# Kernel tuning notes

Measured on AMD Instinct MI355X. Metric: run time of the kernel, lower is better.

Reference implementation:

```python
import jax, jax.numpy as jnp
import numpy as np

B, S, H, NH = 8, 1024, 1024, 4
D = H // NH
NEG = jnp.float32(-2**32 + 1)


def setup_inputs() -> dict:
    key = jax.random.key(0)
    ks = jax.random.split(key, 12)
    w = 1.0 / np.sqrt(H)
    wf = 1.0 / np.sqrt(2 * H)
    return {
        "memory": jax.random.normal(ks[0], (B, S, H), jnp.float32),
        "decoder_input": jax.random.normal(ks[1], (B, S, H), jnp.float32),
        "mask": jax.random.bernoulli(ks[2], 0.2, (B, S, S)),
        "query_mask": (jax.random.uniform(ks[3], (B, S)) > 0.1).astype(jnp.float32),
        "Wk": jax.random.normal(ks[4], (H, H), jnp.float32) * w,
        "Wv": jax.random.normal(ks[5], (H, H), jnp.float32) * w,
        "Wq": jax.random.normal(ks[6], (H, H), jnp.float32) * w,
        "Wf": jax.random.normal(ks[7], (2 * H, H), jnp.float32) * wf,
        "bf": jnp.zeros((H,), jnp.float32),
        "gamma": jnp.ones((H,), jnp.float32),
        "beta": jnp.zeros((H,), jnp.float32),
        "g_factor": jax.random.uniform(ks[8], (1,), jnp.float32, 1e4, 2e4),
    }


def reference(memory, decoder_input, mask, query_mask, Wk, Wv, Wq, Wf, bf, gamma, beta, g_factor):
    b, sq, hdim = decoder_input.shape
    sk = memory.shape[1]

    def heads(x, W, s):  # -> (NH, B, s, D), matching torch permute(2,0,1,3)
        return (x @ W).reshape(b, s, NH, D).transpose(2, 0, 1, 3)

    k = heads(memory, Wk, sk)
    v = heads(memory, Wv, sk)
    q = heads(decoder_input, Wq, sq)

    attn = jnp.einsum("hbqd,hbkd->hbqk", q, k) / jnp.sqrt(jnp.float32(D))
    idx = jnp.arange(sk, dtype=jnp.float32)
    gauss = (idx[:, None] - idx[None, :]) ** 2 / g_factor[0]  # (sq, sk), sq==sk
    attn = attn - gauss
    attn = jnp.where(mask[None], NEG, attn)
    attn = jax.nn.softmax(attn, axis=-1)
    attn = attn * query_mask[None, :, :, None]  # post-softmax query mask

    res = jnp.einsum("hbqk,hbkd->hbqd", attn, v)
    res = res.transpose(1, 2, 0, 3).reshape(b, sq, hdim)

    out = jnp.concatenate([decoder_input, res], axis=-1) @ Wf + bf
    out = out + decoder_input
    mu = out.mean(-1, keepdims=True)
    var = ((out - mu) ** 2).mean(-1, keepdims=True)
    out = (out - mu) / jnp.sqrt(var + 1e-5) * gamma + beta
    return out, attn.reshape(NH * b, sq, sk)
```

## Files before the change

### kernel.cpp

```cpp
#include <hip/hip_runtime.h>

#define B_ 8
#define S_ 1024
#define H_ 1024
#define NH_ 4
#define D_ 256
#define M_ 8192

typedef unsigned int u32;
typedef unsigned short u16;
typedef __attribute__((ext_vector_type(4))) float f32x4;
typedef __attribute__((ext_vector_type(8))) short s16x8;

__device__ __forceinline__ float bf2f(u16 b) { return __uint_as_float(((u32)b) << 16); }
__device__ __forceinline__ u16 f2bf(float f) {
    u32 x = __float_as_uint(f);
    return (u16)((x + 0x7fffu + ((x >> 16) & 1u)) >> 16);
}

__global__ void init_flags_k(int* fl) { fl[0] = 0; fl[1] = 0; fl[2] = 0; }

__global__ __launch_bounds__(256) void or_mask_k(const u32* __restrict__ m, int* __restrict__ fl) {
    u32 v = m[blockIdx.x * 256 + threadIdx.x];
#pragma unroll
    for (int o = 32; o; o >>= 1) v |= __shfl_xor(v, o, 64);
    if ((threadIdx.x & 63) == 0) atomicOr(fl + 1, (int)v);
}

__global__ void classify_mask_k(int* fl) {
    u32 R = (u32)fl[1];
    int c;
    if (R == 0x3F803F80u)      c = 2;
    else if (R == 0x3F800000u) c = 3;
    else if (R & 0xFFFFFF00u)  c = 0;
    else                       c = 1;
    fl[2] = c;
}

__global__ __launch_bounds__(256) void tcast_k(const float* __restrict__ src, u16* __restrict__ dst,
                                               int R, int C) {
    __shared__ float sb[32][33];
    const int c0 = blockIdx.x * 32, r0 = blockIdx.y * 32;
    const int tx = threadIdx.x & 31, ty = threadIdx.x >> 5;
#pragma unroll
    for (int i = 0; i < 4; i++)
        sb[ty + 8 * i][tx] = src[(size_t)(r0 + ty + 8 * i) * C + c0 + tx];
    __syncthreads();
#pragma unroll
    for (int i = 0; i < 4; i++)
        dst[(size_t)(c0 + ty + 8 * i) * R + r0 + tx] = f2bf(sb[tx][ty + 8 * i]);
}

__global__ __launch_bounds__(256) void castbf_k(const float* __restrict__ src, u16* __restrict__ dst) {
    const int i = blockIdx.x * 256 + threadIdx.x;
    float4 v = ((const float4*)src)[i];
    ushort4 o;
    o.x = f2bf(v.x); o.y = f2bf(v.y); o.z = f2bf(v.z); o.w = f2bf(v.w);
    ((ushort4*)dst)[i] = o;
}

template<int AMODE>
__device__ __forceinline__ void gemm_core(
    const float* __restrict__ A32, const u16* __restrict__ A16, int lda,
    const u16* __restrict__ Bp, int ldb, int K, int m0, int n0,
    short* As, short* Bs, f32x4 acc[4][4])
{
    const int t = threadIdx.x;
    const int lane = t & 63, wave = t >> 6;
    const int wy = wave >> 1, wx = wave & 1;
    const int mq = lane >> 4, ml = lane & 15;
    const int srow = t >> 2, skq = t & 3;

    for (int k0 = 0; k0 < K; k0 += 32) {
        __syncthreads();
#pragma unroll
        for (int it = 0; it < 2; it++) {
            const int row = srow + it * 64;
            const int kk = k0 + skq * 8;
            short* dst = As + row * 40 + skq * 8;
            if (AMODE == 1) {
                *(s16x8*)dst = *(const s16x8*)(A16 + (size_t)(m0 + row) * lda + kk);
            } else {
                if (kk < 1024) {
                    const float* s = A32 + (size_t)(m0 + row) * 1024 + kk;
                    float4 v0 = *(const float4*)s, v1 = *(const float4*)(s + 4);
                    s16x8 p;
                    p[0] = (short)f2bf(v0.x); p[1] = (short)f2bf(v0.y);
                    p[2] = (short)f2bf(v0.z); p[3] = (short)f2bf(v0.w);
                    p[4] = (short)f2bf(v1.x); p[5] = (short)f2bf(v1.y);
                    p[6] = (short)f2bf(v1.z); p[7] = (short)f2bf(v1.w);
                    *(s16x8*)dst = p;
                } else {
                    *(s16x8*)dst = *(const s16x8*)(A16 + (size_t)(m0 + row) * 1024 + (kk - 1024));
                }
            }
        }
#pragma unroll
        for (int it = 0; it < 2; it++) {
            const int row = srow + it * 64;
            *(s16x8*)(Bs + row * 40 + skq * 8) =
                *(const s16x8*)(Bp + (size_t)(n0 + row) * ldb + k0 + skq * 8);
        }
        __syncthreads();
        s16x8 af[4], bfr[4];
#pragma unroll
        for (int i = 0; i < 4; i++) {
            af[i]  = *(s16x8*)(As + (wy * 64 + i * 16 + ml) * 40 + mq * 8);
            bfr[i] = *(s16x8*)(Bs + (wx * 64 + i * 16 + ml) * 40 + mq * 8);
        }
#pragma unroll
        for (int mi = 0; mi < 4; mi++)
#pragma unroll
            for (int ni = 0; ni < 4; ni++)
                acc[mi][ni] = __builtin_amdgcn_mfma_f32_16x16x32_bf16(af[mi], bfr[ni], acc[mi][ni], 0, 0, 0);
    }
}

__global__ __launch_bounds__(256) void gemm_proj_k(const u16* __restrict__ A, const u16* __restrict__ WT,
                                                   u16* __restrict__ C) {
    __shared__ short As[128 * 40];
    __shared__ short Bs[128 * 40];
    const int m0 = blockIdx.y * 128, n0 = blockIdx.x * 128;
    f32x4 acc[4][4];
#pragma unroll
    for (int i = 0; i < 4; i++)
#pragma unroll
        for (int j = 0; j < 4; j++) acc[i][j] = 0;
    gemm_core<1>(nullptr, A, H_, WT, H_, H_, m0, n0, As, Bs, acc);
    const int lane = threadIdx.x & 63, wave = threadIdx.x >> 6;
    const int wy = wave >> 1, wx = wave & 1, mq = lane >> 4, ml = lane & 15;
#pragma unroll
    for (int mi = 0; mi < 4; mi++)
#pragma unroll
        for (int ni = 0; ni < 4; ni++) {
            const int n = n0 + wx * 64 + ni * 16 + ml;
#pragma unroll
            for (int r = 0; r < 4; r++) {
                const int m = m0 + wy * 64 + mi * 16 + mq * 4 + r;
                C[(size_t)m * H_ + n] = f2bf(acc[mi][ni][r]);
            }
        }
}

__global__ __launch_bounds__(256) void gemm_vt_k(const u16* __restrict__ A, const u16* __restrict__ WT,
                                                 u16* __restrict__ VT) {
    __shared__ short As[128 * 40];
    __shared__ short Bs[128 * 40];
    const int m0 = blockIdx.y * 128, n0 = blockIdx.x * 128;
    f32x4 acc[4][4];
#pragma unroll
    for (int i = 0; i < 4; i++)
#pragma unroll
        for (int j = 0; j < 4; j++) acc[i][j] = 0;
    gemm_core<1>(nullptr, A, H_, WT, H_, H_, m0, n0, As, Bs, acc);
    const int lane = threadIdx.x & 63, wave = threadIdx.x >> 6;
    const int wy = wave >> 1, wx = wave & 1, mq = lane >> 4, ml = lane & 15;
#pragma unroll
    for (int mi = 0; mi < 4; mi++)
#pragma unroll
        for (int ni = 0; ni < 4; ni++) {
            const int n = n0 + wx * 64 + ni * 16 + ml;
            const int mbase = m0 + wy * 64 + mi * 16 + mq * 4;
            const int b = mbase >> 10, s = mbase & 1023;
            ushort4 w;
            w.x = f2bf(acc[mi][ni][0]); w.y = f2bf(acc[mi][ni][1]);
            w.z = f2bf(acc[mi][ni][2]); w.w = f2bf(acc[mi][ni][3]);
            *(ushort4*)(VT + ((size_t)(b * 1024 + n)) * 1024 + s) = w;
        }
}

__global__ __launch_bounds__(512, 2) void qk_sm_k(
    const u16* __restrict__ Qb, const u16* __restrict__ Kb,
    const void* __restrict__ mask, const float* __restrict__ gfac,
    const int* __restrict__ fl, const float* __restrict__ qmask,
    float* __restrict__ attn, const u16* __restrict__ VT, u16* __restrict__ resB)
{
    __shared__ short smem[76288];
    short* As = smem;
    short* Bs = smem + 2560;
    short* Ps = smem;
    short* Vs = smem + 65536;
    float* red = (float*)(smem + 75776);

    const int flat = blockIdx.x;
    const int wgid = (flat & 7) * 64 + (flat >> 3);
    const int z = wgid >> 4, m0 = (wgid & 15) * 64;
    const int h = z >> 3, b = z & 7;

    const u16* Aq = Qb + (size_t)b * S_ * H_ + h * D_;
    const u16* Bk = Kb + (size_t)b * S_ * H_ + h * D_;

    const int t = threadIdx.x;
    const int lane = t & 63, wave = t >> 6;
    const int wm = wave >> 2, wn = wave & 3;
    const int mq = lane >> 4, ml = lane & 15;

    f32x4 acc[2][16];
#pragma unroll
    for (int mi = 0; mi < 2; mi++)
#pragma unroll
        for (int nf = 0; nf < 16; nf++) acc[mi][nf] = 0;

    for (int k0 = 0; k0 < D_; k0 += 32) {
        __syncthreads();
        if (t < 256) {
            const int row = t >> 2, kq = t & 3;
            *(s16x8*)(As + row * 40 + kq * 8) =
                *(const s16x8*)(Aq + (size_t)(m0 + row) * H_ + k0 + kq * 8);
        }
#pragma unroll
        for (int it = 0; it < 8; it++) {
            const int c = it * 512 + t;
            const int row = c >> 2, kq = c & 3;
            *(s16x8*)(Bs + row * 40 + kq * 8) =
                *(const s16x8*)(Bk + (size_t)row * H_ + k0 + kq * 8);
        }
        __syncthreads();
        s16x8 af0 = *(s16x8*)(As + (wm * 32 + ml) * 40 + mq * 8);
        s16x8 af1 = *(s16x8*)(As + (wm * 32 + 16 + ml) * 40 + mq * 8);
#pragma unroll
        for (int g4 = 0; g4 < 4; g4++) {
            s16x8 bf4[4];
#pragma unroll
            for (int j = 0; j < 4; j++)
                bf4[j] = *(s16x8*)(Bs + (wn * 256 + (g4 * 4 + j) * 16 + ml) * 40 + mq * 8);
#pragma unroll
            for (int j = 0; j < 4; j++) {
                acc[0][g4 * 4 + j] = __builtin_amdgcn_mfma_f32_16x16x32_bf16(af0, bf4[j], acc[0][g4 * 4 + j], 0, 0, 0);
                acc[1][g4 * 4 + j] = __builtin_amdgcn_mfma_f32_16x16x32_bf16(af1, bf4[j], acc[1][g4 * 4 + j], 0, 0, 0);
            }
        }
    }

    const float ginv = 1.0f / gfac[0];
    const int code = fl[2];
    const size_t zrow = (size_t)z * S_;
    float rmax[2][4], rsum[2][4], scv[2][4];

#pragma unroll
    for (int mi = 0; mi < 2; mi++)
#pragma unroll
        for (int r = 0; r < 4; r++) {
            const int qg = m0 + wm * 32 + mi * 16 + mq * 4 + r;
            const size_t mbase = ((size_t)b * S_ + qg) * S_;
            float mx = -3.0e38f;
#pragma unroll
            for (int nf = 0; nf < 16; nf++) {
                const int kg = wn * 256 + nf * 16 + ml;
                float diff = (float)(qg - kg);
                float val = acc[mi][nf][r] * 0.0625f - diff * diff * ginv;
                int mv;
                if (code == 0)      mv = ((const unsigned char*)mask)[mbase + kg];
                else if (code == 1) mv = ((const int*)mask)[mbase + kg];
                else if (code == 2) mv = (((const u16*)mask)[mbase + kg] != 0);
                else                mv = (((const u32*)mask)[mbase + kg] != 0);
                if (mv) val = -4294967296.0f;
                acc[mi][nf][r] = val;
                mx = fmaxf(mx, val);
            }
            rmax[mi][r] = mx;
        }
#pragma unroll
    for (int o = 1; o < 16; o <<= 1)
#pragma unroll
        for (int mi = 0; mi < 2; mi++)
#pragma unroll
            for (int r = 0; r < 4; r++)
                rmax[mi][r] = fmaxf(rmax[mi][r], __shfl_xor(rmax[mi][r], o, 64));
    if (ml == 0)
#pragma unroll
        for (int mi = 0; mi < 2; mi++)
#pragma unroll
            for (int r = 0; r < 4; r++) red[(wm * 32 + mi * 16 + mq * 4 + r) * 4 + wn] = rmax[mi][r];
    __syncthreads();
#pragma unroll
    for (int mi = 0; mi < 2; mi++)
#pragma unroll
        for (int r = 0; r < 4; r++) {
            const float* rr = red + (wm * 32 + mi * 16 + mq * 4 + r) * 4;
            rmax[mi][r] = fmaxf(fmaxf(rr[0], rr[1]), fmaxf(rr[2], rr[3]));
        }
    __syncthreads();
#pragma unroll
    for (int mi = 0; mi < 2; mi++)
#pragma unroll
        for (int r = 0; r < 4; r++) {
            float s = 0.f;
#pragma unroll
            for (int nf = 0; nf < 16; nf++) {
                float p = __expf(acc[mi][nf][r] - rmax[mi][r]);
                acc[mi][nf][r] = p;
                s += p;
            }
            rsum[mi][r] = s;
        }
#pragma unroll
    for (int o = 1; o < 16; o <<= 1)
#pragma unroll
        for (int mi = 0; mi < 2; mi++)
#pragma unroll
            for (int r = 0; r < 4; r++) rsum[mi][r] += __shfl_xor(rsum[mi][r], o, 64);
    if (ml == 0)
#pragma unroll
        for (int mi = 0; mi < 2; mi++)
#pragma unroll
            for (int r = 0; r < 4; r++) red[(wm * 32 + mi * 16 + mq * 4 + r) * 4 + wn] = rsum[mi][r];
    __syncthreads();
#pragma unroll
    for (int mi = 0; mi < 2; mi++)
#pragma unroll
        for (int r = 0; r < 4; r++) {
            const float* rr = red + (wm * 32 + mi * 16 + mq * 4 + r) * 4;
            const int qg = m0 + wm * 32 + mi * 16 + mq * 4 + r;
            const float s = rr[0] + rr[1] + rr[2] + rr[3];
            scv[mi][r] = qmask[b * S_ + qg] / s;
        }

#pragma unroll
    for (int mi = 0; mi < 2; mi++)
#pragma unroll
        for (int r = 0; r < 4; r++) {
            const int prow = wm * 32 + mi * 16 + mq * 4 + r;
            const int qg = m0 + prow;
            float* gp = attn + (zrow + qg) * S_ + wn * 256 + ml;
            const float sc = scv[mi][r];
#pragma unroll
            for (int nf = 0; nf < 16; nf++) {
                const float v = acc[mi][nf][r] * sc;
                gp[nf * 16] = v;
                const int col = wn * 256 + nf * 16 + ml;
                Ps[prow * 1024 + (col ^ ((prow & 7) << 3))] = (short)f2bf(v);
            }
        }

    const int wr = wave >> 2, wc = wave & 3;
    f32x4 acc2[2][4];
#pragma unroll
    for (int mi = 0; mi < 2; mi++)
#pragma unroll
        for (int ni = 0; ni < 4; ni++) acc2[mi][ni] = 0;

    const u16* Vp = VT + ((size_t)(b * 1024 + h * D_)) * 1024;
    for (int k0 = 0; k0 < S_; k0 += 32) {
        {
            const int row = t >> 1, half = t & 1;
            const u16* s = Vp + (size_t)row * 1024 + k0 + half * 16;
            short* dpt = Vs + row * 40 + half * 16;
            *(s16x8*)dpt       = *(const s16x8*)s;
            *(s16x8*)(dpt + 8) = *(const s16x8*)(s + 8);
        }
        __syncthreads();
        s16x8 pa[2];
#pragma unroll
        for (int mi = 0; mi < 2; mi++) {
            const int prow = wr * 32 + mi * 16 + ml;
            pa[mi] = *(s16x8*)(Ps + prow * 1024 + ((((k0 >> 3) + mq) ^ (prow & 7)) << 3));
        }
#pragma unroll
        for (int ni = 0; ni < 4; ni++) {
            s16x8 vf = *(s16x8*)(Vs + (wc * 64 + ni * 16 + ml) * 40 + mq * 8);
            acc2[0][ni] = __builtin_amdgcn_mfma_f32_16x16x32_bf16(pa[0], vf, acc2[0][ni], 0, 0, 0);
            acc2[1][ni] = __builtin_amdgcn_mfma_f32_16x16x32_bf16(pa[1], vf, acc2[1][ni], 0, 0, 0);
        }
        __syncthreads();
    }

    u16* C = resB + (size_t)b * S_ * H_ + h * D_;
#pragma unroll
    for (int mi = 0; mi < 2; mi++)
#pragma unroll
        for (int ni = 0; ni < 4; ni++) {
            const int n = wc * 64 + ni * 16 + ml;
#pragma unroll
            for (int r = 0; r < 4; r++) {
                const int m = m0 + wr * 32 + mi * 16 + mq * 4 + r;
                C[(size_t)m * H_ + n] = f2bf(acc2[mi][ni][r]);
            }
        }
}

__global__ __launch_bounds__(256) void final_mfma_k(const float* __restrict__ dec, const u16* __restrict__ resB,
                                                    const u16* __restrict__ WfT, const float* __restrict__ bfv,
                                                    u16* __restrict__ tmp) {
    __shared__ short As[128 * 40];
    __shared__ short Bs[128 * 40];
    const int m0 = blockIdx.y * 128, n0 = blockIdx.x * 128;
    f32x4 acc[4][4];
#pragma unroll
    for (int i = 0; i < 4; i++)
#pragma unroll
        for (int j = 0; j < 4; j++) acc[i][j] = 0;
    gemm_core<2>(dec, resB, H_, WfT, 2048, 2048, m0, n0, As, Bs, acc);
    const int lane = threadIdx.x & 63, wave = threadIdx.x >> 6;
    const int wy = wave >> 1, wx = wave & 1, mq = lane >> 4, ml = lane & 15;
#pragma unroll
    for (int mi = 0; mi < 4; mi++)
#pragma unroll
        for (int ni = 0; ni < 4; ni++) {
            const int n = n0 + wx * 64 + ni * 16 + ml;
#pragma unroll
            for (int r = 0; r < 4; r++) {
                const int m = m0 + wy * 64 + mi * 16 + mq * 4 + r;
                float val = acc[mi][ni][r] + bfv[n] + dec[(size_t)m * H_ + n];
                tmp[(size_t)m * H_ + n] = f2bf(val);
            }
        }
}

__global__ __launch_bounds__(256) void ln2_k(const u16* __restrict__ tmp, const float* __restrict__ gm,
                                             const float* __restrict__ bt, float* __restrict__ out) {
    const int m = blockIdx.x, t = threadIdx.x;
    ushort4 u = ((const ushort4*)(tmp + (size_t)m * H_))[t];
    float xa[4] = {bf2f(u.x), bf2f(u.y), bf2f(u.z), bf2f(u.w)};
    float s = 0.f, s2 = 0.f;
#pragma unroll
    for (int i = 0; i < 4; i++) { s += xa[i]; s2 += xa[i] * xa[i]; }
#pragma unroll
    for (int o = 32; o; o >>= 1) { s += __shfl_xor(s, o, 64); s2 += __shfl_xor(s2, o, 64); }
    __shared__ float rs[4], rs2[4];
    if ((t & 63) == 0) { rs[t >> 6] = s; rs2[t >> 6] = s2; }
    __syncthreads();
    s  = rs[0] + rs[1] + rs[2] + rs[3];
    s2 = rs2[0] + rs2[1] + rs2[2] + rs2[3];
    float mu = s * (1.f / 1024.f);
    float var = s2 * (1.f / 1024.f) - mu * mu;
    float rstd = rsqrtf(var + 1e-5f);
    float ov[4];
#pragma unroll
    for (int i = 0; i < 4; i++) {
        int n = t * 4 + i;
        ov[i] = (xa[i] - mu) * rstd * gm[n] + bt[n];
    }
    *(float4*)(out + (size_t)m * H_ + t * 4) = make_float4(ov[0], ov[1], ov[2], ov[3]);
}

extern "C" void kernel_launch(void* const* d_in, const int* in_sizes, int n_in,
                              void* d_out, int out_size, void* d_ws, size_t ws_size,
                              hipStream_t stream) {
    const float* memory = (const float*)d_in[0];
    const float* dec    = (const float*)d_in[1];
    const void*  mask   = d_in[2];
    const float* qmask  = (const float*)d_in[3];
    const float* Wk     = (const float*)d_in[4];
    const float* Wv     = (const float*)d_in[5];
    const float* Wq     = (const float*)d_in[6];
    const float* Wf     = (const float*)d_in[7];
    const float* bfv    = (const float*)d_in[8];
    const float* gamma  = (const float*)d_in[9];
    const float* beta   = (const float*)d_in[10];
    const float* gfac   = (const float*)d_in[11];

    char* ws = (char*)d_ws;
    int* fl  = (int*)ws;
    u16* WqT = (u16*)(ws + (1u  << 20));
    u16* WkT = (u16*)(ws + (3u  << 20));
    u16* WvT = (u16*)(ws + (5u  << 20));
    u16* WfT = (u16*)(ws + (7u  << 20));
    u16* Qb  = (u16*)(ws + (11u << 20));
    u16* Kb  = (u16*)(ws + (27u << 20));
    u16* VT  = (u16*)(ws + (43u << 20));
    u16* tmpB = Qb;

    float* out   = (float*)d_out;
    float* attnF = out + (size_t)B_ * S_ * H_;

    u16* resB = (u16*)out;

    u16* memB = (u16*)attnF;
    u16* decB = memB + (size_t)B_ * S_ * H_;

    init_flags_k<<<1, 1, 0, stream>>>(fl);
    or_mask_k<<<256, 256, 0, stream>>>((const u32*)mask, fl);
    classify_mask_k<<<1, 1, 0, stream>>>(fl);

    tcast_k<<<dim3(32, 32), 256, 0, stream>>>(Wq, WqT, 1024, 1024);
    tcast_k<<<dim3(32, 32), 256, 0, stream>>>(Wk, WkT, 1024, 1024);
    tcast_k<<<dim3(32, 32), 256, 0, stream>>>(Wv, WvT, 1024, 1024);
    tcast_k<<<dim3(32, 64), 256, 0, stream>>>(Wf, WfT, 2048, 1024);

    castbf_k<<<8192, 256, 0, stream>>>(memory, memB);
    castbf_k<<<8192, 256, 0, stream>>>(dec,    decB);

    gemm_proj_k<<<dim3(8, 64), 256, 0, stream>>>(decB, WqT, Qb);
    gemm_proj_k<<<dim3(8, 64), 256, 0, stream>>>(memB, WkT, Kb);
    gemm_vt_k  <<<dim3(8, 64), 256, 0, stream>>>(memB, WvT, VT);

    qk_sm_k<<<512, 512, 0, stream>>>(Qb, Kb, mask, gfac, fl, qmask, attnF, VT, resB);
    final_mfma_k<<<dim3(8, 64), 256, 0, stream>>>(dec, resB, WfT, bfv, tmpB);
    ln2_k<<<M_, 256, 0, stream>>>(tmpB, gamma, beta, out);
}
```

Baseline: 616.7 us.

## Write decoder bf16 and attention result into one concat buffer for final GEMM

```diff
diff --git a/kernel.cpp b/kernel.cpp
--- a/kernel.cpp
+++ b/kernel.cpp
@@ -59,9 +59,16 @@
     ((ushort4*)dst)[i] = o;
 }
 
-template<int AMODE>
+__global__ __launch_bounds__(256) void castbf2_k(const float* __restrict__ src, u16* __restrict__ dst) {
+    const int m = blockIdx.x, t = threadIdx.x;
+    float4 v = ((const float4*)(src + (size_t)m * 1024))[t];
+    ushort4 o;
+    o.x = f2bf(v.x); o.y = f2bf(v.y); o.z = f2bf(v.z); o.w = f2bf(v.w);
+    *(ushort4*)(dst + (size_t)m * 2048 + t * 4) = o;
+}
+
 __device__ __forceinline__ void gemm_core(
-    const float* __restrict__ A32, const u16* __restrict__ A16, int lda,
+    const u16* __restrict__ A16, int lda,
     const u16* __restrict__ Bp, int ldb, int K, int m0, int n0,
     short* As, short* Bs, f32x4 acc[4][4])
 {
@@ -77,29 +84,10 @@
         for (int it = 0; it < 2; it++) {
             const int row = srow + it * 64;
             const int kk = k0 + skq * 8;
-            short* dst = As + row * 40 + skq * 8;
-            if (AMODE == 1) {
-                *(s16x8*)dst = *(const s16x8*)(A16 + (size_t)(m0 + row) * lda + kk);
-            } else {
-                if (kk < 1024) {
-                    const float* s = A32 + (size_t)(m0 + row) * 1024 + kk;
-                    float4 v0 = *(const float4*)s, v1 = *(const float4*)(s + 4);
-                    s16x8 p;
-                    p[0] = (short)f2bf(v0.x); p[1] = (short)f2bf(v0.y);
-                    p[2] = (short)f2bf(v0.z); p[3] = (short)f2bf(v0.w);
-                    p[4] = (short)f2bf(v1.x); p[5] = (short)f2bf(v1.y);
-                    p[6] = (short)f2bf(v1.z); p[7] = (short)f2bf(v1.w);
-                    *(s16x8*)dst = p;
-                } else {
-                    *(s16x8*)dst = *(const s16x8*)(A16 + (size_t)(m0 + row) * 1024 + (kk - 1024));
-                }
-            }
-        }
-#pragma unroll
-        for (int it = 0; it < 2; it++) {
-            const int row = srow + it * 64;
+            *(s16x8*)(As + row * 40 + skq * 8) =
+                *(const s16x8*)(A16 + (size_t)(m0 + row) * lda + kk);
             *(s16x8*)(Bs + row * 40 + skq * 8) =
-                *(const s16x8*)(Bp + (size_t)(n0 + row) * ldb + k0 + skq * 8);
+                *(const s16x8*)(Bp + (size_t)(n0 + row) * ldb + kk);
         }
         __syncthreads();
         s16x8 af[4], bfr[4];
@@ -116,8 +104,8 @@
     }
 }
 
-__global__ __launch_bounds__(256) void gemm_proj_k(const u16* __restrict__ A, const u16* __restrict__ WT,
-                                                   u16* __restrict__ C) {
+__global__ __launch_bounds__(256) void gemm_proj_k(const u16* __restrict__ A, int lda,
+                                                   const u16* __restrict__ WT, u16* __restrict__ C) {
     __shared__ short As[128 * 40];
     __shared__ short Bs[128 * 40];
     const int m0 = blockIdx.y * 128, n0 = blockIdx.x * 128;
@@ -126,7 +114,7 @@
     for (int i = 0; i < 4; i++)
 #pragma unroll
         for (int j = 0; j < 4; j++) acc[i][j] = 0;
-    gemm_core<1>(nullptr, A, H_, WT, H_, H_, m0, n0, As, Bs, acc);
+    gemm_core(A, lda, WT, H_, H_, m0, n0, As, Bs, acc);
     const int lane = threadIdx.x & 63, wave = threadIdx.x >> 6;
     const int wy = wave >> 1, wx = wave & 1, mq = lane >> 4, ml = lane & 15;
 #pragma unroll
@@ -142,8 +130,8 @@
         }
 }
 
-__global__ __launch_bounds__(256) void gemm_vt_k(const u16* __restrict__ A, const u16* __restrict__ WT,
-                                                 u16* __restrict__ VT) {
+__global__ __launch_bounds__(256) void gemm_vt_k(const u16* __restrict__ A, int lda,
+                                                 const u16* __restrict__ WT, u16* __restrict__ VT) {
     __shared__ short As[128 * 40];
     __shared__ short Bs[128 * 40];
     const int m0 = blockIdx.y * 128, n0 = blockIdx.x * 128;
@@ -152,7 +140,7 @@
     for (int i = 0; i < 4; i++)
 #pragma unroll
         for (int j = 0; j < 4; j++) acc[i][j] = 0;
-    gemm_core<1>(nullptr, A, H_, WT, H_, H_, m0, n0, As, Bs, acc);
+    gemm_core(A, lda, WT, H_, H_, m0, n0, As, Bs, acc);
     const int lane = threadIdx.x & 63, wave = threadIdx.x >> 6;
     const int wy = wave >> 1, wx = wave & 1, mq = lane >> 4, ml = lane & 15;
 #pragma unroll
@@ -173,14 +161,14 @@
     const u16* __restrict__ Qb, const u16* __restrict__ Kb,
     const void* __restrict__ mask, const float* __restrict__ gfac,
     const int* __restrict__ fl, const float* __restrict__ qmask,
-    float* __restrict__ attn, const u16* __restrict__ VT, u16* __restrict__ resB)
+    float* __restrict__ attn, const u16* __restrict__ VT, u16* __restrict__ catB)
 {
-    __shared__ short smem[76288];
+    __shared__ short smem[76544];
     short* As = smem;
     short* Bs = smem + 2560;
     short* Ps = smem;
-    short* Vs = smem + 65536;
-    float* red = (float*)(smem + 75776);
+    short* Vs = smem + 65792;
+    float* red = (float*)(smem + 76032);
 
     const int flat = blockIdx.x;
     const int wgid = (flat & 7) * 64 + (flat >> 3);
@@ -328,8 +316,7 @@
             for (int nf = 0; nf < 16; nf++) {
                 const float v = acc[mi][nf][r] * sc;
                 gp[nf * 16] = v;
-                const int col = wn * 256 + nf * 16 + ml;
-                Ps[prow * 1024 + (col ^ ((prow & 7) << 3))] = (short)f2bf(v);
+                Ps[prow * 1028 + wn * 256 + nf * 16 + ml] = (short)f2bf(v);
             }
         }
 
@@ -354,7 +341,7 @@
 #pragma unroll
         for (int mi = 0; mi < 2; mi++) {
             const int prow = wr * 32 + mi * 16 + ml;
-            pa[mi] = *(s16x8*)(Ps + prow * 1024 + ((((k0 >> 3) + mq) ^ (prow & 7)) << 3));
+            pa[mi] = *(s16x8*)(Ps + prow * 1028 + k0 + mq * 8);
         }
 #pragma unroll
         for (int ni = 0; ni < 4; ni++) {
@@ -365,7 +352,7 @@
         __syncthreads();
     }
 
-    u16* C = resB + (size_t)b * S_ * H_ + h * D_;
+    u16* C = catB + ((size_t)b * S_) * 2048 + 1024 + h * D_;
 #pragma unroll
     for (int mi = 0; mi < 2; mi++)
 #pragma unroll
@@ -374,12 +361,12 @@
 #pragma unroll
             for (int r = 0; r < 4; r++) {
                 const int m = m0 + wr * 32 + mi * 16 + mq * 4 + r;
-                C[(size_t)m * H_ + n] = f2bf(acc2[mi][ni][r]);
-            }
-        }
-}
-
-__global__ __launch_bounds__(256) void final_mfma_k(const float* __restrict__ dec, const u16* __restrict__ resB,
+                C[(size_t)m * 2048 + n] = f2bf(acc2[mi][ni][r]);
+            }
+        }
+}
+
+__global__ __launch_bounds__(256) void final_mfma_k(const float* __restrict__ dec, const u16* __restrict__ catB,
                                                     const u16* __restrict__ WfT, const float* __restrict__ bfv,
                                                     u16* __restrict__ tmp) {
     __shared__ short As[128 * 40];
@@ -390,7 +377,7 @@
     for (int i = 0; i < 4; i++)
 #pragma unroll
         for (int j = 0; j < 4; j++) acc[i][j] = 0;
-    gemm_core<2>(dec, resB, H_, WfT, 2048, 2048, m0, n0, As, Bs, acc);
+    gemm_core(catB, 2048, WfT, 2048, 2048, m0, n0, As, Bs, acc);
     const int lane = threadIdx.x & 63, wave = threadIdx.x >> 6;
     const int wy = wave >> 1, wx = wave & 1, mq = lane >> 4, ml = lane & 15;
 #pragma unroll
@@ -464,10 +451,9 @@
     float* out   = (float*)d_out;
     float* attnF = out + (size_t)B_ * S_ * H_;
 
-    u16* resB = (u16*)out;
+    u16* catB = (u16*)out;
 
     u16* memB = (u16*)attnF;
-    u16* decB = memB + (size_t)B_ * S_ * H_;
 
     init_flags_k<<<1, 1, 0, stream>>>(fl);
     or_mask_k<<<256, 256, 0, stream>>>((const u32*)mask, fl);
@@ -478,14 +464,14 @@
     tcast_k<<<dim3(32, 32), 256, 0, stream>>>(Wv, WvT, 1024, 1024);
     tcast_k<<<dim3(32, 64), 256, 0, stream>>>(Wf, WfT, 2048, 1024);
 
-    castbf_k<<<8192, 256, 0, stream>>>(memory, memB);
-    castbf_k<<<8192, 256, 0, stream>>>(dec,    decB);
-
-    gemm_proj_k<<<dim3(8, 64), 256, 0, stream>>>(decB, WqT, Qb);
-    gemm_proj_k<<<dim3(8, 64), 256, 0, stream>>>(memB, WkT, Kb);
-    gemm_vt_k  <<<dim3(8, 64), 256, 0, stream>>>(memB, WvT, VT);
-
-    qk_sm_k<<<512, 512, 0, stream>>>(Qb, Kb, mask, gfac, fl, qmask, attnF, VT, resB);
-    final_mfma_k<<<dim3(8, 64), 256, 0, stream>>>(dec, resB, WfT, bfv, tmpB);
+    castbf_k <<<8192, 256, 0, stream>>>(memory, memB);
+    castbf2_k<<<8192, 256, 0, stream>>>(dec, catB);
+
+    gemm_proj_k<<<dim3(8, 64), 256, 0, stream>>>(catB, 2048, WqT, Qb);
+    gemm_proj_k<<<dim3(8, 64), 256, 0, stream>>>(memB, 1024, WkT, Kb);
+    gemm_vt_k  <<<dim3(8, 64), 256, 0, stream>>>(memB, 1024, WvT, VT);
+
+    qk_sm_k<<<512, 512, 0, stream>>>(Qb, Kb, mask, gfac, fl, qmask, attnF, VT, catB);
+    final_mfma_k<<<dim3(8, 64), 256, 0, stream>>>(dec, catB, WfT, bfv, tmpB);
     ln2_k<<<M_, 256, 0, stream>>>(tmpB, gamma, beta, out);
 }
```

Result: no change. 617.4 us (+0.1%).
